# Performance work log

Hardware: AMD Instinct MI355X
Metric: run time of the kernel (lower is better)

Reference implementation:

```python
import jax, jax.numpy as jnp
import numpy as np

N_HEAD = 16

def _phi(x):
    # silu(x) + 1 feature map
    return jax.nn.silu(x) + 1.0

def setup_inputs() -> dict:
    key = jax.random.key(0)
    ks = jax.random.split(key, 8)
    B, T, D = 8, 4096, 1024
    s = 0.02
    return {
        "x":  jax.random.normal(ks[0], (B, T, D), jnp.float32),
        "Wq": jax.random.normal(ks[1], (D, D), jnp.float32) * s,
        "bq": jax.random.normal(ks[2], (D,), jnp.float32) * s,
        "Wk": jax.random.normal(ks[3], (D, D), jnp.float32) * s,
        "Wv": jax.random.normal(ks[4], (D, D), jnp.float32) * s,
        "bv": jax.random.normal(ks[5], (D,), jnp.float32) * s,
        "Wo": jax.random.normal(ks[6], (D, D), jnp.float32) * s,
        "bo": jax.random.normal(ks[7], (D,), jnp.float32) * s,
    }

def reference(x, Wq, bq, Wk, Wv, bv, Wo, bo):
    B, T, D = x.shape
    H = N_HEAD
    Dh = D // H
    scale = Dh ** (-0.25)
    # projections (torch F.linear: x @ W.T + b); key has no bias
    q = x @ Wq.T + bq
    k = x @ Wk.T
    v = x @ Wv.T + bv
    # [B, T, H, Dh] -> [B, H, T, Dh]
    q = q.reshape(B, T, H, Dh).transpose(0, 2, 1, 3) * scale
    k = k.reshape(B, T, H, Dh).transpose(0, 2, 1, 3) * scale
    v = v.reshape(B, T, H, Dh).transpose(0, 2, 1, 3)
    phi_q = _phi(q)
    phi_k = _phi(k)
    # kv: [B, H, Dh, Dh] = sum_t phi_k[t]^T v[t]
    kv = jnp.einsum('bhtd,bhte->bhde', phi_k, v)
    out = jnp.einsum('bhtd,bhde->bhte', phi_q, kv)  # [B, H, T, Dh]
    wv = out.transpose(0, 2, 1, 3).reshape(B, T, D)
    return wv @ Wo.T + bo
```

## Files before the change

kernel.cpp:

```cpp
#include <hip/hip_runtime.h>
#include <math.h>

typedef short bf16x8 __attribute__((ext_vector_type(8)));
typedef float f32x4  __attribute__((ext_vector_type(4)));

__device__ __forceinline__ float phi_act(float t) {
    return t / (1.0f + __expf(-t)) + 1.0f;
}

__device__ __forceinline__ unsigned short f2bf(float f) {
    union { float f; unsigned int u; } un; un.f = f;
    unsigned int r = un.u + 0x7fffu + ((un.u >> 16) & 1u);
    return (unsigned short)(r >> 16);
}

__device__ __forceinline__ void gload_lds16(const void* g, void* l) {
    __builtin_amdgcn_global_load_lds(
        (const __attribute__((address_space(1))) void*)g,
        (__attribute__((address_space(3))) void*)l, 16, 0, 0);
}


__device__ __forceinline__ void stage2(const char* g, int voff0, int voff1,
                                       char* l, int wb16) {
    gload_lds16(g + voff0, l + wb16);
    gload_lds16(g + voff1, l + 8192 + wb16);
}

#define LOAD_AF(buf, ah) do {                                                   \
    const char* _s = (const char*)&As[buf][ah][0];                              \
    _Pragma("unroll")                                                           \
    for (int _mi = 0; _mi < 4; _mi++) {                                         \
        const int _row = qm * 64 + _mi * 16 + ml;                               \
        const int _sw = (_row & 7) << 4;                                        \
        _Pragma("unroll")                                                       \
        for (int _ks = 0; _ks < 2; _ks++)                                       \
            af[_mi][_ks] = *(const bf16x8*)(_s +                                \
                (((_row * 128) + _ks * 64 + kq * 16) ^ _sw));                   \
    }                                                                           \
} while (0)

#define LOAD_BF_TO(dst, buf, bh) do {                                           \
    const char* _s = (const char*)&Bs[buf][bh][0];                              \
    _Pragma("unroll")                                                           \
    for (int _nj = 0; _nj < 2; _nj++) {                                         \
        const int _col = qn * 32 + _nj * 16 + ml;                               \
        const int _sw = (_col & 7) << 4;                                        \
        _Pragma("unroll")                                                       \
        for (int _ks = 0; _ks < 2; _ks++)                                       \
            dst[_nj][_ks] = *(const bf16x8*)(_s +                               \
                (((_col * 128) + _ks * 64 + kq * 16) ^ _sw));                   \
    }                                                                           \
} while (0)

#define MFMA_Q(Q, B) do {                                                       \
    __builtin_amdgcn_s_setprio(1);                                              \
    _Pragma("unroll")                                                           \
    for (int _mi = 0; _mi < 4; _mi++)                                           \
        _Pragma("unroll")                                                       \
        for (int _nj = 0; _nj < 2; _nj++)                                       \
            _Pragma("unroll")                                                   \
            for (int _ks = 0; _ks < 2; _ks++)                                   \
                acc[Q][_mi][_nj] = __builtin_amdgcn_mfma_f32_16x16x32_bf16(     \
                    af[_mi][_ks], B[_nj][_ks], acc[Q][_mi][_nj], 0, 0, 0);      \
    __builtin_amdgcn_s_setprio(0);                                              \
} while (0)

template<int KIND>
__device__ __forceinline__ void gemm256_body(
    const unsigned short* __restrict__ A, const unsigned short* __restrict__ W,
    const float* __restrict__ bq, const float* __restrict__ bv,
    unsigned short* __restrict__ oq, unsigned short* __restrict__ okk,
    unsigned short* __restrict__ ov, float* __restrict__ outF,
    const float* __restrict__ bo, float scale, int NBN)
{
    __shared__ __align__(128) unsigned short As[2][2][128 * 64];
    __shared__ __align__(128) unsigned short Bs[2][2][128 * 64];

    const int tid  = threadIdx.x;
    const int lane = tid & 63;
    const int w    = tid >> 6;
    const int qm   = w >> 2;
    const int qn   = w & 3;
    const int ml   = lane & 15;
    const int kq   = lane >> 4;

    const int nwg  = (int)gridDim.x;
    const int bid  = (int)blockIdx.x;
    const int sbid = (bid & 7) * (nwg >> 3) + (bid >> 3);
    const int bn   = sbid % NBN;
    const int bm   = sbid / NBN;

    const char* pA = (const char*)(A + (size_t)bm * 256 * 1024);
    const char* pB = (const char*)(W + (size_t)bn * 256 * 1024);

    int voff[2];
    #pragma unroll
    for (int u = 0; u < 2; u++) {
        const int p  = (u * 512 + tid) * 16;
        const int qq = p ^ (((p >> 7) & 7) << 4);
        voff[u] = (qq >> 7) * 2048 + (qq & 127);
    }
    const int wb16 = (tid & ~63) * 16;

    f32x4 acc[4][4][2];
    f32x4 zero4 = {0.f, 0.f, 0.f, 0.f};
    #pragma unroll
    for (int q = 0; q < 4; q++)
        #pragma unroll
        for (int mi = 0; mi < 4; mi++)
            #pragma unroll
            for (int nj = 0; nj < 2; nj++) acc[q][mi][nj] = zero4;

    bf16x8 af[4][2], bf0[2][2], bf1[2][2];

    stage2(pA,              voff[0], voff[1], (char*)&As[0][0][0], wb16);
    stage2(pB,              voff[0], voff[1], (char*)&Bs[0][0][0], wb16);
    stage2(pB + 256 * 1024, voff[0], voff[1], (char*)&Bs[0][1][0], wb16);
    stage2(pA + 256 * 1024, voff[0], voff[1], (char*)&As[0][1][0], wb16);

    for (int t = 0; t < 16; ++t) {
        const int buf = t & 1;
        const char* A0n = pA + (size_t)(t + 1) * 128;
        const char* A1n = A0n + 256 * 1024;
        const char* B0n = pB + (size_t)(t + 1) * 128;
        const char* B1n = B0n + 256 * 1024;
        const bool st = (t + 1 < 16);

        asm volatile("s_waitcnt vmcnt(4)" ::: "memory");
        __builtin_amdgcn_s_barrier();
        asm volatile("" ::: "memory");
        LOAD_AF(buf, 0);
        LOAD_BF_TO(bf0, buf, 0);
        if (st) {
            stage2(A0n, voff[0], voff[1], (char*)&As[buf ^ 1][0][0], wb16);
            stage2(B0n, voff[0], voff[1], (char*)&Bs[buf ^ 1][0][0], wb16);
        }
        asm volatile("s_waitcnt lgkmcnt(0)" ::: "memory");
        MFMA_Q(0, bf0);

        if (st) { asm volatile("s_waitcnt vmcnt(6)" ::: "memory"); }
        else    { asm volatile("s_waitcnt vmcnt(2)" ::: "memory"); }
        __builtin_amdgcn_s_barrier();
        asm volatile("" ::: "memory");
        LOAD_BF_TO(bf1, buf, 1);
        if (st) stage2(B1n, voff[0], voff[1], (char*)&Bs[buf ^ 1][1][0], wb16);
        asm volatile("s_waitcnt lgkmcnt(0)" ::: "memory");
        MFMA_Q(1, bf1);

        if (st) { asm volatile("s_waitcnt vmcnt(6)" ::: "memory"); }
        else    { asm volatile("s_waitcnt vmcnt(0)" ::: "memory"); }
        __builtin_amdgcn_s_barrier();
        asm volatile("" ::: "memory");
        LOAD_AF(buf, 1);
        if (st) stage2(A1n, voff[0], voff[1], (char*)&As[buf ^ 1][1][0], wb16);
        asm volatile("s_waitcnt lgkmcnt(0)" ::: "memory");
        MFMA_Q(2, bf1);

        MFMA_Q(3, bf0);
    }

    const int rq = lane >> 4, cl = lane & 15;
    #pragma unroll
    for (int q = 0; q < 4; q++) {
        const int qr = (q >> 1) * 128;
        const int qc = ((q == 1) || (q == 2)) ? 128 : 0;
        #pragma unroll
        for (int nj = 0; nj < 2; nj++) {
            const int colg = bn * 256 + qc + qn * 32 + nj * 16 + cl;
            if constexpr (KIND == 0) {
                const int z    = colg >> 10;
                const int lcol = colg & 1023;
                const float bias = (z == 0) ? bq[lcol] : ((z == 2) ? bv[lcol] : 0.f);
                unsigned short* dst = (z == 0) ? oq : ((z == 1) ? okk : ov);
                #pragma unroll
                for (int mi = 0; mi < 4; mi++) {
                    const int row0 = bm * 256 + qr + qm * 64 + mi * 16 + rq * 4;
                    #pragma unroll
                    for (int r = 0; r < 4; r++) {
                        float vv = acc[q][mi][nj][r] + bias;
                        if (z < 2) vv = phi_act(vv * scale);
                        dst[(size_t)(row0 + r) * 1024 + lcol] = f2bf(vv);
                    }
                }
            } else {
                const float bias = bo[colg];
                #pragma unroll
                for (int mi = 0; mi < 4; mi++) {
                    const int row0 = bm * 256 + qr + qm * 64 + mi * 16 + rq * 4;
                    #pragma unroll
                    for (int r = 0; r < 4; r++)
                        outF[(size_t)(row0 + r) * 1024 + colg] = acc[q][mi][nj][r] + bias;
                }
            }
        }
    }
}

__global__ __launch_bounds__(512, 2) void qkv_gemm256(
    const unsigned short* __restrict__ xb,
    const unsigned short* __restrict__ wcat,
    const float* __restrict__ bq, const float* __restrict__ bv,
    unsigned short* __restrict__ phiq, unsigned short* __restrict__ phik,
    unsigned short* __restrict__ vb, float scale)
{
    gemm256_body<0>(xb, wcat, bq, bv, phiq, phik, vb, nullptr, nullptr, scale, 12);
}

__global__ __launch_bounds__(512, 2) void out_gemm256(
    const unsigned short* __restrict__ A, const unsigned short* __restrict__ W,
    const float* __restrict__ bo, float* __restrict__ out)
{
    gemm256_body<1>(A, W, nullptr, nullptr, nullptr, nullptr, nullptr, out, bo, 1.0f, 4);
}

__global__ __launch_bounds__(256) void cast_all(
    const float* __restrict__ x,  unsigned short* __restrict__ xb,
    const float* __restrict__ w0, unsigned short* __restrict__ w0b,
    const float* __restrict__ w1, unsigned short* __restrict__ w1b,
    const float* __restrict__ w2, unsigned short* __restrict__ w2b,
    const float* __restrict__ w3, unsigned short* __restrict__ w3b,
    size_t nx, size_t nw)
{
    size_t i = ((size_t)blockIdx.x * 256 + threadIdx.x) * 4;
    const float* s; unsigned short* d; size_t off;
    if (i < nx)               { s = x;  d = xb;  off = i; }
    else if (i < nx + nw)     { s = w0; d = w0b; off = i - nx; }
    else if (i < nx + 2 * nw) { s = w1; d = w1b; off = i - nx - nw; }
    else if (i < nx + 3 * nw) { s = w2; d = w2b; off = i - nx - 2 * nw; }
    else                      { s = w3; d = w3b; off = i - nx - 3 * nw; }
    float4 v = *(const float4*)(s + off);
    ushort4 o;
    o.x = f2bf(v.x); o.y = f2bf(v.y); o.z = f2bf(v.z); o.w = f2bf(v.w);
    *(ushort4*)(d + off) = o;
}

__global__ __launch_bounds__(256) void kv_part(
    const unsigned short* __restrict__ phiK, const unsigned short* __restrict__ V,
    float* __restrict__ partial, int Ttot, int D)
{
    const int tc = blockIdx.x, bh = blockIdx.y;
    const int b = bh >> 4, h = bh & 15;
    const int tbase = tc * 512;

    __shared__ unsigned short pkT[64][72];
    __shared__ unsigned short vvT[64][72];

    const int tid  = threadIdx.x;
    const int lane = tid & 63;
    const int w    = tid >> 6;
    const int dq = w >> 1, eq = w & 1;
    const int kq = lane >> 4, ml = lane & 15;

    f32x4 zero4 = {0.f, 0.f, 0.f, 0.f};
    f32x4 acc[2][2];
    acc[0][0] = zero4; acc[0][1] = zero4; acc[1][0] = zero4; acc[1][1] = zero4;

    const size_t base = (size_t)b * Ttot * D + h * 64;

    for (int c8 = 0; c8 < 8; c8++) {
        const int t0 = tbase + c8 * 64;
        __syncthreads();
        #pragma unroll
        for (int u = 0; u < 2; u++) {
            const int f = tid * 2 + u;
            const int trow = f >> 3;
            const int d8 = (f & 7) * 8;
            const size_t g = base + (size_t)(t0 + trow) * D + d8;
            uint4 kk = *(const uint4*)(phiK + g);
            uint4 vv = *(const uint4*)(V + g);
            pkT[d8 + 0][trow] = (unsigned short)(kk.x & 0xffff);
            pkT[d8 + 1][trow] = (unsigned short)(kk.x >> 16);
            pkT[d8 + 2][trow] = (unsigned short)(kk.y & 0xffff);
            pkT[d8 + 3][trow] = (unsigned short)(kk.y >> 16);
            pkT[d8 + 4][trow] = (unsigned short)(kk.z & 0xffff);
            pkT[d8 + 5][trow] = (unsigned short)(kk.z >> 16);
            pkT[d8 + 6][trow] = (unsigned short)(kk.w & 0xffff);
            pkT[d8 + 7][trow] = (unsigned short)(kk.w >> 16);
            vvT[d8 + 0][trow] = (unsigned short)(vv.x & 0xffff);
            vvT[d8 + 1][trow] = (unsigned short)(vv.x >> 16);
            vvT[d8 + 2][trow] = (unsigned short)(vv.y & 0xffff);
            vvT[d8 + 3][trow] = (unsigned short)(vv.y >> 16);
            vvT[d8 + 4][trow] = (unsigned short)(vv.z & 0xffff);
            vvT[d8 + 5][trow] = (unsigned short)(vv.z >> 16);
            vvT[d8 + 6][trow] = (unsigned short)(vv.w & 0xffff);
            vvT[d8 + 7][trow] = (unsigned short)(vv.w >> 16);
        }
        __syncthreads();

        #pragma unroll
        for (int ks = 0; ks < 2; ks++) {
            bf16x8 af[2], bfv[2];
            #pragma unroll
            for (int ai = 0; ai < 2; ai++)
                af[ai] = *(const bf16x8*)&pkT[dq * 32 + ai * 16 + ml][ks * 32 + kq * 8];
            #pragma unroll
            for (int bi = 0; bi < 2; bi++)
                bfv[bi] = *(const bf16x8*)&vvT[eq * 32 + bi * 16 + ml][ks * 32 + kq * 8];
            #pragma unroll
            for (int ai = 0; ai < 2; ai++)
                #pragma unroll
                for (int bi = 0; bi < 2; bi++)
                    acc[ai][bi] = __builtin_amdgcn_mfma_f32_16x16x32_bf16(
                        af[ai], bfv[bi], acc[ai][bi], 0, 0, 0);
        }
    }

    float* outp = partial + ((size_t)bh * 8 + tc) * 4096;
    const int rq = lane >> 4, cl = lane & 15;
    #pragma unroll
    for (int ai = 0; ai < 2; ai++)
        #pragma unroll
        for (int bi = 0; bi < 2; bi++) {
            const int e = eq * 32 + bi * 16 + cl;
            #pragma unroll
            for (int r = 0; r < 4; r++) {
                const int d = dq * 32 + ai * 16 + rq * 4 + r;
                outp[d * 64 + e] = acc[ai][bi][r];
            }
        }
}

__global__ __launch_bounds__(256) void kv_reduce(
    const float* __restrict__ partial, unsigned short* __restrict__ kvT)
{
    const int bh = blockIdx.x;
    const int tid = threadIdx.x;
    __shared__ float s[64][65];
    float a[16];
    #pragma unroll
    for (int c = 0; c < 16; c++) a[c] = 0.f;
    #pragma unroll
    for (int p = 0; p < 8; p++) {
        const float* src = partial + ((size_t)bh * 8 + p) * 4096;
        #pragma unroll
        for (int c = 0; c < 16; c++) a[c] += src[c * 256 + tid];
    }
    #pragma unroll
    for (int c = 0; c < 16; c++) {
        const int idx = c * 256 + tid;
        s[idx >> 6][idx & 63] = a[c];
    }
    __syncthreads();
    unsigned short* outp = kvT + (size_t)bh * 4096;
    #pragma unroll
    for (int c = 0; c < 16; c++) {
        const int j = c * 256 + tid;
        outp[j] = f2bf(s[j & 63][j >> 6]);
    }
}

__global__ __launch_bounds__(256) void av_mfma(
    const unsigned short* __restrict__ phiQ, const unsigned short* __restrict__ kvT,
    unsigned short* __restrict__ Oattn, int Ttot, int D)
{
    const int bh = blockIdx.y;
    const int b = bh >> 4, h = bh & 15;
    const int t0 = blockIdx.x * 256;

    __shared__ unsigned short Aq[256 * 64];
    __shared__ unsigned short Kv[64][72];

    const int tid  = threadIdx.x;
    const int lane = tid & 63;
    const int w    = tid >> 6;
    const int kq = lane >> 4, ml = lane & 15;

    {
        const int e = tid >> 2;
        const int c16 = (tid & 3) * 16;
        const unsigned short* src = kvT + (size_t)bh * 4096 + e * 64 + c16;
        *(uint4*)&Kv[e][c16]     = *(const uint4*)(src);
        *(uint4*)&Kv[e][c16 + 8] = *(const uint4*)(src + 8);
    }
    {
        const int lr = lane >> 3;
        const int d8 = (lane & 7) * 8;
        #pragma unroll
        for (int r = 0; r < 8; r++) {
            const int chunk = r * 4 + w;
            const int row = chunk * 8 + lr;
            gload_lds16(phiQ + ((size_t)(b * Ttot + t0 + row)) * D + h * 64 + d8,
                        &Aq[chunk * 512]);
        }
    }
    __syncthreads();

    f32x4 zero4 = {0.f, 0.f, 0.f, 0.f};
    f32x4 acc[4][4];
    #pragma unroll
    for (int i = 0; i < 4; i++)
        #pragma unroll
        for (int j = 0; j < 4; j++) acc[i][j] = zero4;

    #pragma unroll
    for (int ks = 0; ks < 2; ks++) {
        bf16x8 af[4], bfv[4];
        #pragma unroll
        for (int mi = 0; mi < 4; mi++)
            af[mi] = *(const bf16x8*)&Aq[(w * 64 + mi * 16 + ml) * 64 + ks * 32 + kq * 8];
        #pragma unroll
        for (int nj = 0; nj < 4; nj++)
            bfv[nj] = *(const bf16x8*)&Kv[nj * 16 + ml][ks * 32 + kq * 8];
        #pragma unroll
        for (int mi = 0; mi < 4; mi++)
            #pragma unroll
            for (int nj = 0; nj < 4; nj++)
                acc[mi][nj] = __builtin_amdgcn_mfma_f32_16x16x32_bf16(
                    af[mi], bfv[nj], acc[mi][nj], 0, 0, 0);
    }

    const int rq = lane >> 4, cl = lane & 15;
    #pragma unroll
    for (int mi = 0; mi < 4; mi++) {
        #pragma unroll
        for (int r = 0; r < 4; r++) {
            const int t = t0 + w * 64 + mi * 16 + rq * 4 + r;
            unsigned short* dst = Oattn + (size_t)(b * Ttot + t) * D + h * 64;
            #pragma unroll
            for (int nj = 0; nj < 4; nj++)
                dst[nj * 16 + cl] = f2bf(acc[mi][nj][r]);
        }
    }
}

extern "C" void kernel_launch(void* const* d_in, const int* in_sizes, int n_in,
                              void* d_out, int out_size, void* d_ws, size_t ws_size,
                              hipStream_t stream) {
    const float* x  = (const float*)d_in[0];
    const float* Wq = (const float*)d_in[1];
    const float* bq = (const float*)d_in[2];
    const float* Wk = (const float*)d_in[3];
    const float* Wv = (const float*)d_in[4];
    const float* bv = (const float*)d_in[5];
    const float* Wo = (const float*)d_in[6];
    const float* bo = (const float*)d_in[7];
    float* out = (float*)d_out;

    const int B = 8, T = 4096, D = 1024;
    const int M = B * T;
    const float scale = 0.35355339059327379f;
    const size_t MD = (size_t)M * D;
    const size_t WN = (size_t)D * D;

    unsigned short* xb    = (unsigned short*)d_ws;
    unsigned short* wqb   = xb + MD;
    unsigned short* wkb   = wqb + WN;
    unsigned short* wvb   = wkb + WN;
    unsigned short* wob   = wvb + WN;
    unsigned short* phiq  = wob + WN;
    unsigned short* phik  = phiq + MD;
    unsigned short* vb    = phik + MD;
    unsigned short* oat   = vb + MD;
    float*          part  = (float*)(oat + MD);
    unsigned short* kvT   = (unsigned short*)(part + (size_t)1024 * 4096);
    (void)ws_size; (void)in_sizes; (void)n_in; (void)out_size;

    dim3 blk(256);

    {
        size_t total4 = (MD + 4 * WN) / 4;
        cast_all<<<dim3((unsigned)(total4 / 256)), blk, 0, stream>>>(
            x, xb, Wq, wqb, Wk, wkb, Wv, wvb, Wo, wob, MD, WN);
    }

    qkv_gemm256<<<dim3(1536), dim3(512), 0, stream>>>(
        xb, wqb, bq, bv, phiq, phik, vb, scale);

    kv_part<<<dim3(8, 128), blk, 0, stream>>>(phik, vb, part, T, D);
    kv_reduce<<<dim3(128), blk, 0, stream>>>(part, kvT);

    av_mfma<<<dim3(T / 256, 128), blk, 0, stream>>>(phiq, kvT, oat, T, D);

    out_gemm256<<<dim3(512), dim3(512), 0, stream>>>(oat, wob, bo, out);
}
```

Before: 608.9 us.

## Restructure GEMM main loop into barrier-bracketed ping-pong phases around each MFMA quadrant

Reorganizes the double-buffered 256x256 GEMM loop so that every MFMA quadrant is bracketed by two barriers, with LDS fragment reads and global-to-LDS stages issued before the first barrier and the vmcnt waits re-placed. This resembles the ping-pong scheduling used with s_setprio, which aligns waves so that memory issue and MFMA phases alternate across waves. It adds extra barriers per iteration and changes wait counts, which risks more stalls or ordering hazards if the counts are wrong.

Result: slower. 630.3 us (+3.5%).

```diff
diff --git a/kernel.cpp b/kernel.cpp
--- a/kernel.cpp
+++ b/kernel.cpp
@@ -66,6 +66,18 @@
     __builtin_amdgcn_s_setprio(0);                                              \
 } while (0)
 
+#define BARRIER_A() do {                                                        \
+    asm volatile("" ::: "memory");                                              \
+    __builtin_amdgcn_s_barrier();                                               \
+    asm volatile("s_waitcnt lgkmcnt(0)" ::: "memory");                          \
+} while (0)
+
+#define BARRIER_B() do {                                                        \
+    asm volatile("" ::: "memory");                                              \
+    __builtin_amdgcn_s_barrier();                                               \
+    asm volatile("" ::: "memory");                                              \
+} while (0)
+
 template<int KIND>
 __device__ __forceinline__ void gemm256_body(
     const unsigned short* __restrict__ A, const unsigned short* __restrict__ W,
@@ -118,6 +130,8 @@
     stage2(pB,              voff[0], voff[1], (char*)&Bs[0][0][0], wb16);
     stage2(pB + 256 * 1024, voff[0], voff[1], (char*)&Bs[0][1][0], wb16);
     stage2(pA + 256 * 1024, voff[0], voff[1], (char*)&As[0][1][0], wb16);
+    asm volatile("s_waitcnt vmcnt(4)" ::: "memory");
+    BARRIER_B();
 
     for (int t = 0; t < 16; ++t) {
         const int buf = t & 1;
@@ -127,37 +141,40 @@
         const char* B1n = B0n + 256 * 1024;
         const bool st = (t + 1 < 16);
 
-        asm volatile("s_waitcnt vmcnt(4)" ::: "memory");
-        __builtin_amdgcn_s_barrier();
-        asm volatile("" ::: "memory");
         LOAD_AF(buf, 0);
         LOAD_BF_TO(bf0, buf, 0);
         if (st) {
             stage2(A0n, voff[0], voff[1], (char*)&As[buf ^ 1][0][0], wb16);
+            asm volatile("s_waitcnt vmcnt(4)" ::: "memory");
+        } else {
+            asm volatile("s_waitcnt vmcnt(2)" ::: "memory");
+        }
+        BARRIER_A();
+        MFMA_Q(0, bf0);
+        BARRIER_B();
+
+        LOAD_BF_TO(bf1, buf, 1);
+        if (st) {
             stage2(B0n, voff[0], voff[1], (char*)&Bs[buf ^ 1][0][0], wb16);
-        }
-        asm volatile("s_waitcnt lgkmcnt(0)" ::: "memory");
-        MFMA_Q(0, bf0);
-
-        if (st) { asm volatile("s_waitcnt vmcnt(6)" ::: "memory"); }
-        else    { asm volatile("s_waitcnt vmcnt(2)" ::: "memory"); }
-        __builtin_amdgcn_s_barrier();
-        asm volatile("" ::: "memory");
-        LOAD_BF_TO(bf1, buf, 1);
+            asm volatile("s_waitcnt vmcnt(4)" ::: "memory");
+        } else {
+            asm volatile("s_waitcnt vmcnt(0)" ::: "memory");
+        }
+        BARRIER_A();
+        MFMA_Q(1, bf1);
+        BARRIER_B();
+
+        LOAD_AF(buf, 1);
         if (st) stage2(B1n, voff[0], voff[1], (char*)&Bs[buf ^ 1][1][0], wb16);
-        asm volatile("s_waitcnt lgkmcnt(0)" ::: "memory");
-        MFMA_Q(1, bf1);
-
-        if (st) { asm volatile("s_waitcnt vmcnt(6)" ::: "memory"); }
-        else    { asm volatile("s_waitcnt vmcnt(0)" ::: "memory"); }
-        __builtin_amdgcn_s_barrier();
-        asm volatile("" ::: "memory");
-        LOAD_AF(buf, 1);
+        BARRIER_A();
+        MFMA_Q(2, bf1);
+        BARRIER_B();
+
         if (st) stage2(A1n, voff[0], voff[1], (char*)&As[buf ^ 1][1][0], wb16);
-        asm volatile("s_waitcnt lgkmcnt(0)" ::: "memory");
-        MFMA_Q(2, bf1);
-
+        asm volatile("s_waitcnt vmcnt(4)" ::: "memory");
+        BARRIER_A();
         MFMA_Q(3, bf0);
+        BARRIER_B();
     }
 
     const int rq = lane >> 4, cl = lane & 15;
```
